# Kernel tuning notes

Hardware: AMD Instinct MI355X
Metric: run time of the kernel (lower is better)

## Reference

```python
import jax, jax.numpy as jnp
import numpy as np

N = 20000    # num nodes
E = 320000   # num edges (also rows of edge_type, SPN line-graph style)
F = 64       # num_features
HID = 64     # hidden_channels
HEADS = 4    # gatv2_heads
NC = 2       # num_classes
PH = 128     # proxy hidden size
SLOPE = 0.2  # PyG GATv2 leaky_relu negative slope


def gatv2(feat, src, dst, wl, wr, att, b, num_nodes, concat):
    # GATv2Conv (PyG semantics, add_self_loops=True, dropout off in eval)
    H, C = att.shape
    xl = (feat @ wl).reshape(-1, H, C)
    xr = (feat @ wr).reshape(-1, H, C)
    loops = jnp.arange(num_nodes, dtype=src.dtype)
    s = jnp.concatenate([src, loops])
    d = jnp.concatenate([dst, loops])
    e = jax.nn.leaky_relu(xl[s] + xr[d], SLOPE)            # [E', H, C]
    logits = jnp.einsum('ehc,hc->eh', e, att)              # [E', H]
    m = jax.ops.segment_max(logits, d, num_segments=num_nodes)
    p = jnp.exp(logits - m[d])
    z = jax.ops.segment_sum(p, d, num_segments=num_nodes)
    alpha = p / z[d]                                       # segment softmax
    out = jax.ops.segment_sum(xl[s] * alpha[:, :, None], d, num_segments=num_nodes)
    out = out.reshape(num_nodes, H * C) if concat else out.mean(axis=1)
    return out + b


def setup_inputs():
    key = jax.random.key(0)
    ks = iter(jax.random.split(key, 32))
    def rn(shape, scale=0.1):
        return jax.random.normal(next(ks), shape, dtype=jnp.float32) * scale
    return {
        'x': rn((N, F), 1.0),
        'edge_type': rn((E, F), 1.0),
        'edge_index': jax.random.randint(next(ks), (2, E), 0, N, dtype=jnp.int32),
        'n1_wl': rn((F, HEADS * HID)), 'n1_wr': rn((F, HEADS * HID)),
        'n1_att': rn((HEADS, HID)), 'n1_b': jnp.zeros((HEADS * HID,), jnp.float32),
        'n2_wl': rn((HEADS * HID, HID)), 'n2_wr': rn((HEADS * HID, HID)),
        'n2_att': rn((1, HID)), 'n2_b': jnp.zeros((HID,), jnp.float32),
        'e1_wl': rn((F, HEADS * HID)), 'e1_wr': rn((F, HEADS * HID)),
        'e1_att': rn((HEADS, HID)), 'e1_b': jnp.zeros((HEADS * HID,), jnp.float32),
        'e2_wl': rn((HEADS * HID, HID)), 'e2_wr': rn((HEADS * HID, HID)),
        'e2_att': rn((1, HID)), 'e2_b': jnp.zeros((HID,), jnp.float32),
        'crf_wu': rn((HID, NC)), 'crf_bu': jnp.zeros((NC,), jnp.float32),
        'crf_wp': rn((HID, NC)),
        'px_w1': rn((HID, PH)), 'px_b1': jnp.zeros((PH,), jnp.float32),
        'px_w2': rn((PH, NC)), 'px_b2': jnp.zeros((NC,), jnp.float32),
    }


def reference(x, edge_type, edge_index, n1_wl, n1_wr, n1_att, n1_b, n2_wl, n2_wr, n2_att, n2_b,
              e1_wl, e1_wr, e1_att, e1_b, e2_wl, e2_wr, e2_att, e2_b,
              crf_wu, crf_bu, crf_wp, px_w1, px_b1, px_w2, px_b2):
    src, dst = edge_index[0], edge_index[1]
    # node GNN: GATv2 -> ELU -> GATv2 (dropout = identity in eval)
    h = jax.nn.elu(gatv2(x, src, dst, n1_wl, n1_wr, n1_att, n1_b, N, True))
    node_repr = gatv2(h, src, dst, n2_wl, n2_wr, n2_att, n2_b, N, False)
    # edge GNN over edge features (E rows, same edge_index, per source code)
    g = jax.nn.elu(gatv2(edge_type, src, dst, e1_wl, e1_wr, e1_att, e1_b, E, True))
    edge_repr = gatv2(g, src, dst, e2_wl, e2_wr, e2_att, e2_b, E, False)
    # CRF head: unary potentials + pairwise messages scattered to dst nodes
    unary = node_repr @ crf_wu + crf_bu
    msg = jax.ops.segment_sum(edge_repr @ crf_wp, dst, num_segments=N)
    crf_out = jax.nn.log_softmax(unary + msg, axis=-1)
    # MLP proxy head
    ph = jax.nn.relu(node_repr @ px_w1 + px_b1)
    proxy_out = ph @ px_w2 + px_b2
    return crf_out, proxy_out
```

## Files before the change

### kernel.cpp

```cpp
#include <hip/hip_runtime.h>
#include <cstddef>
#include <cstdint>

#define N_NODES 20000
#define N_EDGES 320000

typedef __attribute__((ext_vector_type(8))) short bf8_t;
typedef __attribute__((ext_vector_type(4))) float f4_t;
typedef __attribute__((ext_vector_type(2))) float f2_t;
typedef unsigned short bfu;
typedef _Float16 half_t;
typedef __attribute__((ext_vector_type(2))) _Float16 h2_t;
typedef __attribute__((ext_vector_type(4))) _Float16 h4_t;
typedef __attribute__((ext_vector_type(8))) _Float16 h8_t;

__device__ __forceinline__ short f2bf(float f) {
  unsigned u = __float_as_uint(f);
  u += 0x7fff + ((u >> 16) & 1);
  return (short)(u >> 16);
}
__device__ __forceinline__ h2_t abs_h2(h2_t t) {
  unsigned u = __builtin_bit_cast(unsigned, t) & 0x7fff7fffu;
  return __builtin_bit_cast(h2_t, u);
}
__device__ __forceinline__ float dot2h(h2_t a, h2_t b, float c) {
#if __has_builtin(__builtin_amdgcn_fdot2)
  return __builtin_amdgcn_fdot2(a, b, c, false);
#else
  return c + (float)a.x * (float)b.x + (float)a.y * (float)b.y;
#endif
}

__global__ void count_deg_kernel(const int* __restrict__ dst, int* __restrict__ deg, int e_cnt) {
  int e = blockIdx.x * blockDim.x + threadIdx.x;
  if (e < e_cnt) atomicAdd(&deg[dst[e]], 1);
}

__global__ __launch_bounds__(1024) void scan_kernel(
    const int* __restrict__ deg, int* __restrict__ rowptr,
    int* __restrict__ cursor, int n) {
  __shared__ int sdata[1024];
  constexpr int CH = (N_NODES + 1023) / 1024;
  int tid = threadIdx.x;
  int base = tid * CH;
  int loc[CH];
  int s = 0;
  #pragma unroll
  for (int j = 0; j < CH; ++j) {
    int idx = base + j;
    int v = (idx < n) ? deg[idx] : 0;
    loc[j] = s;
    s += v;
  }
  sdata[tid] = s;
  __syncthreads();
  for (int off = 1; off < 1024; off <<= 1) {
    int t = (tid >= off) ? sdata[tid - off] : 0;
    __syncthreads();
    sdata[tid] += t;
    __syncthreads();
  }
  int excl = sdata[tid] - s;
  #pragma unroll
  for (int j = 0; j < CH; ++j) {
    int idx = base + j;
    if (idx < n) { int val = excl + loc[j]; rowptr[idx] = val; cursor[idx] = val; }
  }
  if (tid == 0) rowptr[n] = sdata[1023];
}

__global__ void fill_csr_kernel(const int* __restrict__ src, const int* __restrict__ dst,
                                int* __restrict__ cursor, int* __restrict__ csr_src,
                                int* __restrict__ csr_eid, int e_cnt) {
  int e = blockIdx.x * blockDim.x + threadIdx.x;
  if (e < e_cnt) {
    int pos = atomicAdd(&cursor[dst[e]], 1);
    csr_src[pos] = src[e];
    csr_eid[pos] = e;
  }
}

__global__ void prep_all_kernel(
    const float* __restrict__ n1l, const float* __restrict__ n1r,
    const float* __restrict__ e1l, const float* __restrict__ e1r,
    const float* __restrict__ n2l, const float* __restrict__ n2r,
    const float* __restrict__ e2l, const float* __restrict__ e2r,
    const float* __restrict__ b2, const float* __restrict__ wp,
    short* __restrict__ t_n1l, short* __restrict__ t_n1r,
    short* __restrict__ t_e1l, short* __restrict__ t_e1r,
    short* __restrict__ t_n2l, short* __restrict__ t_n2r,
    short* __restrict__ t_e2l, short* __restrict__ t_e2r,
    float* __restrict__ wct, float* __restrict__ pc)
{
  int i = blockIdx.x * blockDim.x + threadIdx.x;
  int seg = i >> 14;
  int j = i & 16383;
  if (seg < 4) {
    const float* srcs[4] = {n1l, n1r, e1l, e1r};
    short* dsts[4] = {t_n1l, t_n1r, t_e1l, t_e1r};
    int n = j >> 6, k = j & 63;
    dsts[seg][n * 64 + k] = f2bf(srcs[seg][k * 256 + n]);
  } else if (seg < 8) {
    const float* srcs[4] = {n2l, n2r, e2l, e2r};
    short* dsts[4] = {t_n2l, t_n2r, t_e2l, t_e2r};
    int n = j >> 8, k = j & 255;
    dsts[seg - 4][n * 256 + k] = f2bf(srcs[seg - 4][k * 64 + n]);
  } else if (seg == 8) {
    if (j < 512) {
      int jj = j & 1;
      int k  = j >> 1;
      float s = 0.f;
      for (int c = 0; c < 64; ++c) s = fmaf(e2l[k * 64 + c], wp[c * 2 + jj], s);
      wct[jj * 256 + k] = s;
    } else if (j < 514) {
      int jj = j - 512;
      float s = 0.f;
      for (int c = 0; c < 64; ++c) s = fmaf(b2[c], wp[c * 2 + jj], s);
      pc[jj] = s;
    }
  }
}

template<int K, typename SrcT>
__global__ __launch_bounds__(128) void mfma_proj2_kernel(
    const SrcT* __restrict__ A0,
    const short* __restrict__ Wtl0, const short* __restrict__ Wtr0,
    half_t* __restrict__ xl0, half_t* __restrict__ xr0,
    const SrcT* __restrict__ A1,
    const short* __restrict__ Wtl1, const short* __restrict__ Wtr1,
    half_t* __restrict__ xl1, half_t* __restrict__ xr1,
    const float* __restrict__ att0, const float* __restrict__ att1,
    float* __restrict__ ll0, float* __restrict__ lr0,
    float* __restrict__ ll1, float* __restrict__ lr1,
    int M, int nslices)
{
  constexpr int KC = K / 32;
  int tid = threadIdx.x;
  int w = tid >> 6, lane = tid & 63, quad = lane >> 4, l15 = lane & 15;
  int row_base = (int)blockIdx.x * 64 + w * 32;
  int y = (int)blockIdx.y;
  int z = (int)blockIdx.z;
  const SrcT* A = z ? A1 : A0;
  bool is_l = y < nslices;
  const short* Wt = z ? (is_l ? Wtl1 : Wtr1) : (is_l ? Wtl0 : Wtr0);
  half_t* dst = z ? (is_l ? xl1 : xr1) : (is_l ? xl0 : xr0);
  const float* att = z ? att1 : att0;
  float* lin = z ? (is_l ? ll1 : lr1) : (is_l ? ll0 : lr0);
  int head = is_l ? y : y - nslices;
  int cb = head * 64;
  const float* atp = att + head * 64;
  int STR = nslices * 64;

  bf8_t a[2][KC];
  #pragma unroll
  for (int rt = 0; rt < 2; ++rt) {
    int r = row_base + rt * 16 + l15;
    int rc = r < M ? r : M - 1;
    const SrcT* ap = A + (size_t)rc * K + quad * 8;
    #pragma unroll
    for (int kc = 0; kc < KC; ++kc) {
      bf8_t f;
      if constexpr (sizeof(SrcT) == 4) {
        float4 v0 = *(const float4*)(ap + kc * 32);
        float4 v1 = *(const float4*)(ap + kc * 32 + 4);
        f[0] = f2bf(v0.x); f[1] = f2bf(v0.y); f[2] = f2bf(v0.z); f[3] = f2bf(v0.w);
        f[4] = f2bf(v1.x); f[5] = f2bf(v1.y); f[6] = f2bf(v1.z); f[7] = f2bf(v1.w);
      } else {
        h8_t hv = *(const h8_t*)(ap + kc * 32);
        #pragma unroll
        for (int q = 0; q < 8; ++q) f[q] = f2bf((float)hv[q]);
      }
      a[rt][kc] = f;
    }
  }

  float lacc0 = 0.f, lacc1 = 0.f;
  #pragma unroll
  for (int nt = 0; nt < 4; ++nt) {
    f4_t acc0 = {0.f, 0.f, 0.f, 0.f};
    f4_t acc1 = {0.f, 0.f, 0.f, 0.f};
    const short* wb = Wt + (size_t)(cb + nt * 16 + l15) * K + quad * 8;
    #pragma unroll
    for (int kc = 0; kc < KC; ++kc) {
      bf8_t wf = *(const bf8_t*)(wb + kc * 32);
      acc0 = __builtin_amdgcn_mfma_f32_16x16x32_bf16(wf, a[0][kc], acc0, 0, 0, 0);
      acc1 = __builtin_amdgcn_mfma_f32_16x16x32_bf16(wf, a[1][kc], acc1, 0, 0, 0);
    }
    f4_t av = *(const f4_t*)(atp + nt * 16 + quad * 4);
    lacc0 += acc0[0] * av[0] + acc0[1] * av[1] + acc0[2] * av[2] + acc0[3] * av[3];
    lacc1 += acc1[0] * av[0] + acc1[1] * av[1] + acc1[2] * av[2] + acc1[3] * av[3];
    #pragma unroll
    for (int rt = 0; rt < 2; ++rt) {
      f4_t acc = rt == 0 ? acc0 : acc1;
      int row = row_base + rt * 16 + l15;
      if (row >= M) continue;
      int col = cb + nt * 16 + quad * 4;
      h4_t pk;
      pk[0] = (_Float16)acc[0]; pk[1] = (_Float16)acc[1];
      pk[2] = (_Float16)acc[2]; pk[3] = (_Float16)acc[3];
      *(h4_t*)&dst[(size_t)row * STR + col] = pk;
    }
  }
  lacc0 += __shfl_xor(lacc0, 16, 64); lacc0 += __shfl_xor(lacc0, 32, 64);
  lacc1 += __shfl_xor(lacc1, 16, 64); lacc1 += __shfl_xor(lacc1, 32, 64);
  if (quad == 0) {
    int r0 = row_base + l15;
    int r1 = row_base + 16 + l15;
    if (r0 < M) lin[(size_t)r0 * nslices + head] = 0.6f * lacc0;
    if (r1 < M) lin[(size_t)r1 * nslices + head] = 0.6f * lacc1;
  }
}

template<int KIN>
__device__ __forceinline__ void gemm_body(
    const float* __restrict__ A, const float* __restrict__ W, int wld, int cb,
    int block_m, int M, float (&acc)[8][4],
    float (*As)[128 + 4], float (*Ws)[64 + 4])
{
  int tid = threadIdx.x;
  int tx = tid & 15;
  int ty = tid >> 4;
  #pragma unroll
  for (int i = 0; i < 8; ++i)
    #pragma unroll
    for (int j = 0; j < 4; ++j) acc[i][j] = 0.f;

  for (int k0 = 0; k0 < KIN; k0 += 16) {
    #pragma unroll
    for (int rep = 0; rep < 2; ++rep) {
      int ar = (tid >> 2) + rep * 64;
      int ak = (tid & 3) * 4;
      int gr = block_m + ar;
      float4 v = make_float4(0.f, 0.f, 0.f, 0.f);
      if (gr < M) v = *(const float4*)&A[(size_t)gr * KIN + k0 + ak];
      As[ak + 0][ar] = v.x; As[ak + 1][ar] = v.y;
      As[ak + 2][ar] = v.z; As[ak + 3][ar] = v.w;
    }
    {
      int wr = tid >> 4;
      int wc = (tid & 15) * 4;
      float4 v = *(const float4*)&W[(size_t)(k0 + wr) * wld + cb + wc];
      Ws[wr][wc + 0] = v.x; Ws[wr][wc + 1] = v.y;
      Ws[wr][wc + 2] = v.z; Ws[wr][wc + 3] = v.w;
    }
    __syncthreads();
    #pragma unroll
    for (int k = 0; k < 16; ++k) {
      float a[8], w[4];
      #pragma unroll
      for (int i = 0; i < 8; ++i) a[i] = As[k][ty * 8 + i];
      #pragma unroll
      for (int j = 0; j < 4; ++j) w[j] = Ws[k][tx * 4 + j];
      #pragma unroll
      for (int i = 0; i < 8; ++i)
        #pragma unroll
        for (int j = 0; j < 4; ++j) acc[i][j] = fmaf(a[i], w[j], acc[i][j]);
    }
    __syncthreads();
  }
}

template<int KIN, int MODE>
__global__ __launch_bounds__(256) void gemm64_kernel(
    const float* __restrict__ A, const float* __restrict__ W, int wld,
    const float* __restrict__ bias, float* __restrict__ out, int old, int M)
{
  __shared__ float As[16][128 + 4];
  __shared__ float Ws[16][64 + 4];
  float acc[8][4];
  int block_m = (int)blockIdx.x * 128;
  int cb = (int)blockIdx.y * 64;
  gemm_body<KIN>(A, W, wld, cb, block_m, M, acc, As, Ws);

  int tid = threadIdx.x;
  int tx = tid & 15, ty = tid >> 4;
  int gc = cb + tx * 4;
  #pragma unroll
  for (int i = 0; i < 8; ++i) {
    int gr = block_m + ty * 8 + i;
    if (gr >= M) continue;
    size_t idx = (size_t)gr * old + gc;
    float t0 = acc[i][0], t1 = acc[i][1], t2 = acc[i][2], t3 = acc[i][3];
    if (MODE == 3) {
      t0 = fmaxf(t0 + bias[gc + 0], 0.f);
      t1 = fmaxf(t1 + bias[gc + 1], 0.f);
      t2 = fmaxf(t2 + bias[gc + 2], 0.f);
      t3 = fmaxf(t3 + bias[gc + 3], 0.f);
    }
    *(float4*)&out[idx] = make_float4(t0, t1, t2, t3);
  }
}

__global__ __launch_bounds__(256) void gat_agg_l1(
    const half_t* __restrict__ xl0, const half_t* __restrict__ xr0,
    const float* __restrict__ att0, const float* __restrict__ bias0,
    half_t* __restrict__ out0,
    const half_t* __restrict__ xl1, const half_t* __restrict__ xr1,
    const float* __restrict__ att1, const float* __restrict__ bias1,
    half_t* __restrict__ out1,
    const float* __restrict__ ll0, const float* __restrict__ lr0,
    const float* __restrict__ ll1, const float* __restrict__ lr1,
    const int* __restrict__ rowptr, const int* __restrict__ csr_src)
{
  constexpr int GRP = N_NODES / 4;
  int tid = threadIdx.x;
  int w = tid >> 6, lane = tid & 63;
  int egrp = lane >> 5;
  int head = (lane >> 3) & 3;
  int coff = (lane & 31) * 8;
  int bid = (int)blockIdx.x;
  int chain = bid >= GRP ? 1 : 0;
  int d = (bid - chain * GRP) * 4 + w;

  const half_t* xl = chain ? xl1 : xl0;
  const half_t* xr = chain ? xr1 : xr0;
  const float* att = chain ? att1 : att0;
  const float* bias = chain ? bias1 : bias0;
  const float* linl = chain ? ll1 : ll0;
  const float* linr = chain ? lr1 : lr0;
  half_t* out = chain ? out1 : out0;

  int row0 = rowptr[d];
  int deg = rowptr[d + 1] - row0;

  h2_t xr2[4], attA[4];
  {
    h8_t xv = *(const h8_t*)&xr[(unsigned)(d * 256 + coff)];
    xr2[0] = h2_t{xv[0], xv[1]}; xr2[1] = h2_t{xv[2], xv[3]};
    xr2[2] = h2_t{xv[4], xv[5]}; xr2[3] = h2_t{xv[6], xv[7]};
    const float* atp = att + coff;
    float4 b0 = *(const float4*)(atp);
    float4 b1 = *(const float4*)(atp + 4);
    attA[0] = h2_t{(_Float16)(0.4f * b0.x), (_Float16)(0.4f * b0.y)};
    attA[1] = h2_t{(_Float16)(0.4f * b0.z), (_Float16)(0.4f * b0.w)};
    attA[2] = h2_t{(_Float16)(0.4f * b1.x), (_Float16)(0.4f * b1.y)};
    attA[3] = h2_t{(_Float16)(0.4f * b1.z), (_Float16)(0.4f * b1.w)};
  }
  float linr_d = linr[(unsigned)(d * 4 + head)];

  auto ld_idx = [&](int k) -> int {
    int idx = k * 2 + egrp;
    int cl = idx < deg ? idx : (deg > 0 ? deg - 1 : 0);
    int pos = deg > 0 ? row0 + cl : 0;
    int sv = csr_src[pos];
    return idx < deg ? sv : d;
  };

  float zloc, a8[8];
  {
    h8_t xu = *(const h8_t*)&xl[(unsigned)(d * 256 + coff)];
    float part = 0.f;
    #pragma unroll
    for (int j = 0; j < 4; ++j) {
      h2_t t = h2_t{xu[2 * j], xu[2 * j + 1]} + xr2[j];
      part = dot2h(abs_h2(t), attA[j], part);
    }
    part += __shfl_xor(part, 1, 64);
    part += __shfl_xor(part, 2, 64);
    part += __shfl_xor(part, 4, 64);
    part += linl[(unsigned)(d * 4 + head)] + linr_d;
    float wgt = __expf(part);
    float ws = (egrp == 0) ? wgt : 0.f;
    zloc = ws;
    #pragma unroll
    for (int i = 0; i < 8; ++i) a8[i] = (float)xu[i] * ws;
  }

  int C = (deg + 1) >> 1;
  int s_cur = ld_idx(0);
  h8_t xu_cur = *(const h8_t*)&xl[(unsigned)(s_cur * 256 + coff)];
  float lin_cur = linl[(unsigned)(s_cur * 4 + head)];
  int s_nxt = ld_idx(1);
  for (int k = 0; k < C; ++k) {
    h8_t xu_nxt = *(const h8_t*)&xl[(unsigned)(s_nxt * 256 + coff)];
    float lin_nxt = linl[(unsigned)(s_nxt * 4 + head)];
    int s_n2 = ld_idx(k + 2);
    bool valid = (k * 2 + egrp) < deg;
    float part = 0.f;
    #pragma unroll
    for (int j = 0; j < 4; ++j) {
      h2_t t = h2_t{xu_cur[2 * j], xu_cur[2 * j + 1]} + xr2[j];
      part = dot2h(abs_h2(t), attA[j], part);
    }
    part += __shfl_xor(part, 1, 64);
    part += __shfl_xor(part, 2, 64);
    part += __shfl_xor(part, 4, 64);
    part += lin_cur + linr_d;
    float wgt = valid ? __expf(part) : 0.f;
    zloc += wgt;
    #pragma unroll
    for (int i = 0; i < 8; ++i) a8[i] = fmaf((float)xu_cur[i], wgt, a8[i]);
    xu_cur = xu_nxt; lin_cur = lin_nxt; s_nxt = s_n2;
  }

  zloc += __shfl_xor(zloc, 32, 64);
  #pragma unroll
  for (int i = 0; i < 8; ++i) a8[i] += __shfl_xor(a8[i], 32, 64);

  if (egrp == 0) {
    float invz = 1.f / zloc;
    const float* bp = bias + coff;
    float4 c0 = *(const float4*)(bp);
    float4 c1 = *(const float4*)(bp + 4);
    float o[8];
    o[0] = a8[0] * invz + c0.x; o[1] = a8[1] * invz + c0.y;
    o[2] = a8[2] * invz + c0.z; o[3] = a8[3] * invz + c0.w;
    o[4] = a8[4] * invz + c1.x; o[5] = a8[5] * invz + c1.y;
    o[6] = a8[6] * invz + c1.z; o[7] = a8[7] * invz + c1.w;
    #pragma unroll
    for (int i = 0; i < 8; ++i) o[i] = o[i] > 0.f ? o[i] : __expf(o[i]) - 1.f;
    h8_t pk;
    #pragma unroll
    for (int i = 0; i < 8; ++i) pk[i] = (_Float16)o[i];
    *(h8_t*)&out[(size_t)d * 256 + coff] = pk;
  }
}

__global__ __launch_bounds__(256) void gat_agg_l2(
    const half_t* __restrict__ xl0, const half_t* __restrict__ xr0,
    const float* __restrict__ att0, const float* __restrict__ bias0,
    float* __restrict__ out0,
    const half_t* __restrict__ xl1, const half_t* __restrict__ xr1,
    const float* __restrict__ att1, const float* __restrict__ bias1,
    const float* __restrict__ ll0, const float* __restrict__ lr0,
    const float* __restrict__ ll1, const float* __restrict__ lr1,
    const int* __restrict__ rowptr, const int* __restrict__ csr_src,
    const float* __restrict__ wp, float* __restrict__ pbuf)
{
  constexpr int GRP = N_NODES / 4;
  int tid = threadIdx.x;
  int w = tid >> 6;
  int lane = tid & 63;
  int egrp = lane >> 3;
  int cch  = lane & 7;
  int bid = (int)blockIdx.x;
  int chain = bid >= GRP ? 1 : 0;
  int d = (bid - chain * GRP) * 4 + w;

  const half_t* xl = chain ? xl1 : xl0;
  const half_t* xr = chain ? xr1 : xr0;
  const float* att = chain ? att1 : att0;
  const float* bias = chain ? bias1 : bias0;
  const float* linl = chain ? ll1 : ll0;
  const float* linr = chain ? lr1 : lr0;

  int row0 = rowptr[d];
  int deg = rowptr[d + 1] - row0;
  int cbase = cch * 8;

  h2_t xr2[4], attA[4];
  {
    h8_t xv = *(const h8_t*)&xr[(unsigned)(d * 64 + cbase)];
    xr2[0] = h2_t{xv[0], xv[1]}; xr2[1] = h2_t{xv[2], xv[3]};
    xr2[2] = h2_t{xv[4], xv[5]}; xr2[3] = h2_t{xv[6], xv[7]};
    const float* atp = att + cbase;
    float4 b0 = *(const float4*)(atp);
    float4 b1 = *(const float4*)(atp + 4);
    attA[0] = h2_t{(_Float16)(0.4f * b0.x), (_Float16)(0.4f * b0.y)};
    attA[1] = h2_t{(_Float16)(0.4f * b0.z), (_Float16)(0.4f * b0.w)};
    attA[2] = h2_t{(_Float16)(0.4f * b1.x), (_Float16)(0.4f * b1.y)};
    attA[3] = h2_t{(_Float16)(0.4f * b1.z), (_Float16)(0.4f * b1.w)};
  }
  float linr_d = linr[d];

  auto ld_idx = [&](int k) -> int {
    int idx = k * 8 + egrp;
    int cl = idx < deg ? idx : (deg > 0 ? deg - 1 : 0);
    int pos = deg > 0 ? row0 + cl : 0;
    int sv = csr_src[pos];
    return idx < deg ? sv : d;
  };

  float zloc, a8[8];
  {
    h8_t xu = *(const h8_t*)&xl[(unsigned)(d * 64 + cbase)];
    float part = 0.f;
    #pragma unroll
    for (int j = 0; j < 4; ++j) {
      h2_t t = h2_t{xu[2 * j], xu[2 * j + 1]} + xr2[j];
      part = dot2h(abs_h2(t), attA[j], part);
    }
    part += __shfl_xor(part, 1, 64);
    part += __shfl_xor(part, 2, 64);
    part += __shfl_xor(part, 4, 64);
    part += linl[d] + linr_d;
    float wgt = __expf(part);
    float ws = (egrp == 0) ? wgt : 0.f;
    zloc = ws;
    #pragma unroll
    for (int i = 0; i < 8; ++i) a8[i] = (float)xu[i] * ws;
  }

  int C = (deg + 7) >> 3;
  int s_cur = ld_idx(0);
  h8_t xu_cur = *(const h8_t*)&xl[(unsigned)(s_cur * 64 + cbase)];
  float lin_cur = linl[s_cur];
  int s_nxt = ld_idx(1);
  for (int k = 0; k < C; ++k) {
    h8_t xu_nxt = *(const h8_t*)&xl[(unsigned)(s_nxt * 64 + cbase)];
    float lin_nxt = linl[s_nxt];
    int s_n2 = ld_idx(k + 2);
    bool valid = (k * 8 + egrp) < deg;
    float part = 0.f;
    #pragma unroll
    for (int j = 0; j < 4; ++j) {
      h2_t t = h2_t{xu_cur[2 * j], xu_cur[2 * j + 1]} + xr2[j];
      part = dot2h(abs_h2(t), attA[j], part);
    }
    part += __shfl_xor(part, 1, 64);
    part += __shfl_xor(part, 2, 64);
    part += __shfl_xor(part, 4, 64);
    part += lin_cur + linr_d;
    float wgt = valid ? __expf(part) : 0.f;
    zloc += wgt;
    #pragma unroll
    for (int i = 0; i < 8; ++i) a8[i] = fmaf((float)xu_cur[i], wgt, a8[i]);
    xu_cur = xu_nxt; lin_cur = lin_nxt; s_nxt = s_n2;
  }

  #pragma unroll
  for (int off = 8; off < 64; off <<= 1) {
    zloc += __shfl_xor(zloc, off, 64);
    #pragma unroll
    for (int i = 0; i < 8; ++i) a8[i] += __shfl_xor(a8[i], off, 64);
  }

  float invz = 1.f / zloc;
  float o[8];
  #pragma unroll
  for (int i = 0; i < 8; ++i) o[i] = a8[i] * invz + bias[cbase + i];

  if (chain) {
    float p0 = 0.f, p1 = 0.f;
    #pragma unroll
    for (int i = 0; i < 8; ++i) {
      float2 wv = *(const float2*)&wp[(cbase + i) * 2];
      p0 = fmaf(o[i], wv.x, p0);
      p1 = fmaf(o[i], wv.y, p1);
    }
    p0 += __shfl_xor(p0, 1, 64); p1 += __shfl_xor(p1, 1, 64);
    p0 += __shfl_xor(p0, 2, 64); p1 += __shfl_xor(p1, 2, 64);
    p0 += __shfl_xor(p0, 4, 64); p1 += __shfl_xor(p1, 4, 64);
    if (lane == 0) *(float2*)&pbuf[2 * d] = make_float2(p0, p1);
  } else if (egrp == 0) {
    float* op = out0 + (size_t)d * 64 + cbase;
    *(float4*)(op)     = make_float4(o[0], o[1], o[2], o[3]);
    *(float4*)(op + 4) = make_float4(o[4], o[5], o[6], o[7]);
  }
}

__global__ __launch_bounds__(256) void chunk_fold_kernel(
    const float* __restrict__ A,
    const short* __restrict__ W1t,
    const float* __restrict__ b1,
    const float* __restrict__ WcT,
    const float* __restrict__ pc,
    float* __restrict__ pbufN,
    int Mtot)
{
  __shared__ short Ws[256 * 72];
  __shared__ float b1s[256];
  __shared__ float wcs[512];

  int tid = threadIdx.x;
  int w = tid >> 6;
  int lane = tid & 63;
  int quad = lane >> 4;
  int l15 = lane & 15;
  int row_base = (int)blockIdx.x * 256 + w * 64;

  #pragma unroll
  for (int j = 0; j < 8; ++j) {
    int g = j * 256 + tid;
    int row = g >> 3, c = g & 7;
    *(int4*)&Ws[row * 72 + c * 8] = *(const int4*)&W1t[(size_t)g * 8];
  }
  b1s[tid] = b1[tid];
  wcs[tid] = WcT[tid];
  wcs[256 + tid] = WcT[256 + tid];
  __syncthreads();

  bf8_t a1[4][2];
  #pragma unroll
  for (int rt = 0; rt < 4; ++rt) {
    int r = row_base + rt * 16 + l15;
    int rc = r < Mtot ? r : Mtot - 1;
    const float* ap = A + (size_t)rc * 64 + quad * 8;
    #pragma unroll
    for (int ks = 0; ks < 2; ++ks) {
      float4 v0 = *(const float4*)(ap + ks * 32);
      float4 v1 = *(const float4*)(ap + ks * 32 + 4);
      bf8_t f;
      f[0] = f2bf(v0.x); f[1] = f2bf(v0.y); f[2] = f2bf(v0.z); f[3] = f2bf(v0.w);
      f[4] = f2bf(v1.x); f[5] = f2bf(v1.y); f[6] = f2bf(v1.z); f[7] = f2bf(v1.w);
      a1[rt][ks] = f;
    }
  }

  float p0[4] = {0.f, 0.f, 0.f, 0.f};
  float p1[4] = {0.f, 0.f, 0.f, 0.f};

  #pragma unroll
  for (int i = 0; i < 16; ++i) {
    const short* wl = &Ws[(i * 16 + l15) * 72 + quad * 8];
    bf8_t w0 = *(const bf8_t*)(wl);
    bf8_t w1 = *(const bf8_t*)(wl + 32);

    f4_t g[4];
    #pragma unroll
    for (int rt = 0; rt < 4; ++rt) {
      f4_t z = {0.f, 0.f, 0.f, 0.f};
      z = __builtin_amdgcn_mfma_f32_16x16x32_bf16(w0, a1[rt][0], z, 0, 0, 0);
      z = __builtin_amdgcn_mfma_f32_16x16x32_bf16(w1, a1[rt][1], z, 0, 0, 0);
      g[rt] = z;
    }
    int cbase = i * 16 + quad * 4;
    f4_t b4  = *(const f4_t*)&b1s[cbase];
    f4_t wc0 = *(const f4_t*)&wcs[cbase];
    f4_t wc1 = *(const f4_t*)&wcs[256 + cbase];
    #pragma unroll
    for (int rt = 0; rt < 4; ++rt) {
      #pragma unroll
      for (int r = 0; r < 4; ++r) {
        float v = g[rt][r] + b4[r];
        v = v > 0.f ? v : __expf(v) - 1.f;
        p0[rt] = fmaf(v, wc0[r], p0[rt]);
        p1[rt] = fmaf(v, wc1[r], p1[rt]);
      }
    }
  }

  #pragma unroll
  for (int off = 16; off < 64; off <<= 1) {
    #pragma unroll
    for (int rt = 0; rt < 4; ++rt) {
      p0[rt] += __shfl_xor(p0[rt], off, 64);
      p1[rt] += __shfl_xor(p1[rt], off, 64);
    }
  }
  if (quad == 0) {
    float c0 = pc[0], c1 = pc[1];
    #pragma unroll
    for (int rt = 0; rt < 4; ++rt) {
      int row = row_base + rt * 16 + l15;
      if (row < Mtot)
        *(float2*)&pbufN[2 * row] = make_float2(p0[rt] + c0, p1[rt] + c1);
    }
  }
}

__global__ void head_kernel(const float* __restrict__ node_repr, const float* __restrict__ ph,
                            const int* __restrict__ rowptr, const int* __restrict__ csr_eid,
                            const float* __restrict__ pbuf, const float* __restrict__ wu,
                            const float* __restrict__ bu, const float* __restrict__ w2,
                            const float* __restrict__ b2, float* __restrict__ out, int n) {
  __shared__ float swu[128];
  __shared__ float sw2[256];
  int tid = threadIdx.x;
  if (tid < 128) swu[tid] = wu[tid];
  sw2[tid] = w2[tid];
  __syncthreads();
  int i = blockIdx.x * blockDim.x + tid;
  if (i >= n) return;
  float m0 = 0.f, m1 = 0.f;
  int r0 = rowptr[i], r1 = rowptr[i + 1];
  int jj = r0;
  for (; jj + 4 <= r1; jj += 4) {
    int e0 = csr_eid[jj + 0], e1 = csr_eid[jj + 1];
    int e2 = csr_eid[jj + 2], e3 = csr_eid[jj + 3];
    float2 q0 = *(const float2*)&pbuf[2 * e0];
    float2 q1 = *(const float2*)&pbuf[2 * e1];
    float2 q2 = *(const float2*)&pbuf[2 * e2];
    float2 q3 = *(const float2*)&pbuf[2 * e3];
    m0 += (q0.x + q1.x) + (q2.x + q3.x);
    m1 += (q0.y + q1.y) + (q2.y + q3.y);
  }
  for (; jj < r1; ++jj) {
    int e = csr_eid[jj];
    float2 q = *(const float2*)&pbuf[2 * e];
    m0 += q.x; m1 += q.y;
  }
  const float* nr = node_repr + (size_t)i * 64;
  float u0 = bu[0], u1 = bu[1];
  #pragma unroll
  for (int k = 0; k < 64; ++k) {
    float v = nr[k];
    u0 = fmaf(v, swu[2 * k + 0], u0);
    u1 = fmaf(v, swu[2 * k + 1], u1);
  }
  float v0 = u0 + m0;
  float v1 = u1 + m1;
  float mx = fmaxf(v0, v1);
  float lse = mx + logf(__expf(v0 - mx) + __expf(v1 - mx));
  out[2 * i + 0] = v0 - lse;
  out[2 * i + 1] = v1 - lse;
  const float* p = ph + (size_t)i * 128;
  float p0 = b2[0], p1 = b2[1];
  #pragma unroll
  for (int k = 0; k < 128; ++k) {
    float v = p[k];
    p0 = fmaf(v, sw2[2 * k + 0], p0);
    p1 = fmaf(v, sw2[2 * k + 1], p1);
  }
  out[2 * n + 2 * i + 0] = p0;
  out[2 * n + 2 * i + 1] = p1;
}

extern "C" void kernel_launch(void* const* d_in, const int* in_sizes, int n_in,
                              void* d_out, int out_size, void* d_ws, size_t ws_size,
                              hipStream_t stream) {
  const int N = N_NODES, E = N_EDGES;
  const float* x         = (const float*)d_in[0];
  const float* edge_type = (const float*)d_in[1];
  const int*   ei        = (const int*)d_in[2];
  const float* n1_wl  = (const float*)d_in[3];
  const float* n1_wr  = (const float*)d_in[4];
  const float* n1_att = (const float*)d_in[5];
  const float* n1_b   = (const float*)d_in[6];
  const float* n2_wl  = (const float*)d_in[7];
  const float* n2_wr  = (const float*)d_in[8];
  const float* n2_att = (const float*)d_in[9];
  const float* n2_b   = (const float*)d_in[10];
  const float* e1_wl  = (const float*)d_in[11];
  const float* e1_wr  = (const float*)d_in[12];
  const float* e1_att = (const float*)d_in[13];
  const float* e1_b   = (const float*)d_in[14];
  const float* e2_wl  = (const float*)d_in[15];
  const float* e2_wr  = (const float*)d_in[16];
  const float* e2_att = (const float*)d_in[17];
  const float* e2_b   = (const float*)d_in[18];
  const float* crf_wu = (const float*)d_in[19];
  const float* crf_bu = (const float*)d_in[20];
  const float* crf_wp = (const float*)d_in[21];
  const float* px_w1  = (const float*)d_in[22];
  const float* px_b1  = (const float*)d_in[23];
  const float* px_w2  = (const float*)d_in[24];
  const float* px_b2  = (const float*)d_in[25];
  float* out = (float*)d_out;
  const int* src = ei;
  const int* dst = ei + E;
  (void)in_sizes; (void)n_in; (void)out_size; (void)ws_size;

  char* ws = (char*)d_ws;
  size_t off = 0;
  auto alloc = [&](size_t bytes) -> void* {
    void* p = ws + off;
    off += (bytes + 255) & ~(size_t)255;
    return p;
  };
  half_t* xl_n  = (half_t*)alloc((size_t)N * 256 * 2);
  half_t* xr_n  = (half_t*)alloc((size_t)N * 256 * 2);
  half_t* xl_e  = (half_t*)alloc((size_t)N * 256 * 2);
  half_t* xr_e  = (half_t*)alloc((size_t)N * 256 * 2);
  half_t* h_n  = (half_t*)alloc((size_t)N * 256 * 4);
  half_t* g_e  = (half_t*)alloc((size_t)N * 256 * 4);
  half_t* xl2_n = (half_t*)alloc((size_t)N * 64 * 2);
  half_t* xr2_n = (half_t*)alloc((size_t)N * 64 * 2);
  half_t* xl2_e = (half_t*)alloc((size_t)N * 64 * 2);
  half_t* xr2_e = (half_t*)alloc((size_t)N * 64 * 2);
  float* B3    = (float*)alloc((size_t)N * 64 * 4);
  float* pbuf  = (float*)alloc((size_t)E * 2 * 4);
  float* ph    = (float*)(void*)xl_n;
  int* deg     = (int*)alloc((size_t)N * 4);
  int* rowptr  = (int*)alloc((size_t)(N + 1) * 4);
  int* cursor  = (int*)alloc((size_t)N * 4);
  int* csr_src = (int*)alloc((size_t)E * 4);
  int* csr_eid = (int*)alloc((size_t)E * 4);
  short* t_n1l = (short*)alloc((size_t)16384 * 2);
  short* t_n1r = (short*)alloc((size_t)16384 * 2);
  short* t_e1l = (short*)alloc((size_t)16384 * 2);
  short* t_e1r = (short*)alloc((size_t)16384 * 2);
  short* t_n2l = (short*)alloc((size_t)16384 * 2);
  short* t_n2r = (short*)alloc((size_t)16384 * 2);
  short* t_e2l = (short*)alloc((size_t)16384 * 2);
  short* t_e2r = (short*)alloc((size_t)16384 * 2);
  float* WcT   = (float*)alloc((size_t)2 * 256 * 4);
  float* pcv   = (float*)alloc((size_t)2 * 4);
  float* l1ln = pbuf;
  float* l1rn = pbuf + 80000;
  float* l1le = pbuf + 160000;
  float* l1re = pbuf + 240000;
  float* l2base = (float*)(void*)xr_n;
  float* l2ln = l2base;
  float* l2rn = l2base + 20000;
  float* l2le = l2base + 40000;
  float* l2re = l2base + 60000;

  const int EB = (E + 255) / 256;
  const int NB = (N + 127) / 128;
  const int PB = (N + 63) / 64;
  const int Mhigh = E - N;
  const int CFB = (Mhigh + 255) / 256;
  const int GRP = N / 4;

  hipMemsetAsync(deg, 0, (size_t)N * 4, stream);
  count_deg_kernel<<<EB, 256, 0, stream>>>(dst, deg, E);
  scan_kernel<<<1, 1024, 0, stream>>>(deg, rowptr, cursor, N);
  fill_csr_kernel<<<EB, 256, 0, stream>>>(src, dst, cursor, csr_src, csr_eid, E);
  prep_all_kernel<<<515, 256, 0, stream>>>(n1_wl, n1_wr, e1_wl, e1_wr,
                                           n2_wl, n2_wr, e2_wl, e2_wr,
                                           e2_b, crf_wp,
                                           t_n1l, t_n1r, t_e1l, t_e1r,
                                           t_n2l, t_n2r, t_e2l, t_e2r, WcT, pcv);

  mfma_proj2_kernel<64, float><<<dim3(PB, 8, 2), 128, 0, stream>>>(
      x, t_n1l, t_n1r, xl_n, xr_n,
      edge_type, t_e1l, t_e1r, xl_e, xr_e,
      n1_att, e1_att, l1ln, l1rn, l1le, l1re, N, 4);
  gat_agg_l1<<<2 * GRP, 256, 0, stream>>>(
      xl_n, xr_n, n1_att, n1_b, h_n,
      xl_e, xr_e, e1_att, e1_b, g_e,
      l1ln, l1rn, l1le, l1re, rowptr, csr_src);

  mfma_proj2_kernel<256, half_t><<<dim3(PB, 2, 2), 128, 0, stream>>>(
      h_n, t_n2l, t_n2r, xl2_n, xr2_n,
      g_e, t_e2l, t_e2r, xl2_e, xr2_e,
      n2_att, e2_att, l2ln, l2rn, l2le, l2re, N, 1);
  gat_agg_l2<<<2 * GRP, 256, 0, stream>>>(
      xl2_n, xr2_n, n2_att, n2_b, B3,
      xl2_e, xr2_e, e2_att, e2_b,
      l2ln, l2rn, l2le, l2re, rowptr, csr_src, crf_wp, pbuf);

  chunk_fold_kernel<<<CFB, 256, 0, stream>>>(edge_type + (size_t)N * 64, t_e1l,
                                             e1_b, WcT, pcv, pbuf + 2 * (size_t)N, Mhigh);

  gemm64_kernel<64, 3><<<dim3(NB, 2), 256, 0, stream>>>(B3, px_w1, 128, px_b1, ph, 128, N);
  head_kernel<<<(N + 255) / 256, 256, 0, stream>>>(B3, ph, rowptr, csr_eid, pbuf,
                                                   crf_wu, crf_bu, px_w2, px_b2, out, N);
}
```

Measured before the change: 397.8 us.

## Schedule aggregation nodes in descending-degree order via counting sort

Adds a degree histogram, a scan and a scatter pass that build a permutation of nodes sorted by descending in-degree. Both GAT aggregation kernels then process destination nodes in that order, so heavy nodes start first and the tail of the launch is better balanced. The cost is three extra small kernel launches plus a memset, and the loss of locality between neighbouring destination ids within a block. The order buffer reuses the cursor array and the histogram reuses B3, both of which must already be free at those points.

```diff
diff --git a/kernel.cpp b/kernel.cpp
--- a/kernel.cpp
+++ b/kernel.cpp
@@ -77,6 +77,39 @@
     int pos = atomicAdd(&cursor[dst[e]], 1);
     csr_src[pos] = src[e];
     csr_eid[pos] = e;
+  }
+}
+
+__global__ void deg_hist_kernel(const int* __restrict__ deg, int* __restrict__ hist, int n) {
+  int i = blockIdx.x * blockDim.x + threadIdx.x;
+  if (i < n) {
+    int b = deg[i]; b = b > 511 ? 511 : b;
+    atomicAdd(&hist[511 - b], 1);
+  }
+}
+
+__global__ __launch_bounds__(512) void hist_scan_kernel(
+    const int* __restrict__ hist, int* __restrict__ hcur) {
+  __shared__ int s[512];
+  int t = threadIdx.x;
+  s[t] = hist[t];
+  __syncthreads();
+  for (int off = 1; off < 512; off <<= 1) {
+    int v = (t >= off) ? s[t - off] : 0;
+    __syncthreads();
+    s[t] += v;
+    __syncthreads();
+  }
+  hcur[t] = s[t] - hist[t];
+}
+
+__global__ void order_scatter_kernel(const int* __restrict__ deg, int* __restrict__ hcur,
+                                     int* __restrict__ order, int n) {
+  int i = blockIdx.x * blockDim.x + threadIdx.x;
+  if (i < n) {
+    int b = deg[i]; b = b > 511 ? 511 : b;
+    int pos = atomicAdd(&hcur[511 - b], 1);
+    order[pos] = i;
   }
 }
 
@@ -300,7 +333,8 @@
     half_t* __restrict__ out1,
     const float* __restrict__ ll0, const float* __restrict__ lr0,
     const float* __restrict__ ll1, const float* __restrict__ lr1,
-    const int* __restrict__ rowptr, const int* __restrict__ csr_src)
+    const int* __restrict__ rowptr, const int* __restrict__ csr_src,
+    const int* __restrict__ order)
 {
   constexpr int GRP = N_NODES / 4;
   int tid = threadIdx.x;
@@ -310,7 +344,7 @@
   int coff = (lane & 31) * 8;
   int bid = (int)blockIdx.x;
   int chain = bid >= GRP ? 1 : 0;
-  int d = (bid - chain * GRP) * 4 + w;
+  int d = order[(bid - chain * GRP) * 4 + w];
 
   const half_t* xl = chain ? xl1 : xl0;
   const half_t* xr = chain ? xr1 : xr0;
@@ -425,7 +459,8 @@
     const float* __restrict__ ll0, const float* __restrict__ lr0,
     const float* __restrict__ ll1, const float* __restrict__ lr1,
     const int* __restrict__ rowptr, const int* __restrict__ csr_src,
-    const float* __restrict__ wp, float* __restrict__ pbuf)
+    const float* __restrict__ wp, float* __restrict__ pbuf,
+    const int* __restrict__ order)
 {
   constexpr int GRP = N_NODES / 4;
   int tid = threadIdx.x;
@@ -435,7 +470,7 @@
   int cch  = lane & 7;
   int bid = (int)blockIdx.x;
   int chain = bid >= GRP ? 1 : 0;
-  int d = (bid - chain * GRP) * 4 + w;
+  int d = order[(bid - chain * GRP) * 4 + w];
 
   const half_t* xl = chain ? xl1 : xl0;
   const half_t* xr = chain ? xr1 : xr0;
@@ -785,18 +820,26 @@
   float* l2rn = l2base + 20000;
   float* l2le = l2base + 40000;
   float* l2re = l2base + 60000;
+  int* hist  = (int*)(void*)B3;
+  int* hcur  = hist + 512;
+  int* order = cursor;
 
   const int EB = (E + 255) / 256;
   const int NB = (N + 127) / 128;
   const int PB = (N + 63) / 64;
+  const int NB256 = (N + 255) / 256;
   const int Mhigh = E - N;
   const int CFB = (Mhigh + 255) / 256;
   const int GRP = N / 4;
 
   hipMemsetAsync(deg, 0, (size_t)N * 4, stream);
+  hipMemsetAsync(hist, 0, 512 * 4, stream);
   count_deg_kernel<<<EB, 256, 0, stream>>>(dst, deg, E);
   scan_kernel<<<1, 1024, 0, stream>>>(deg, rowptr, cursor, N);
   fill_csr_kernel<<<EB, 256, 0, stream>>>(src, dst, cursor, csr_src, csr_eid, E);
+  deg_hist_kernel<<<NB256, 256, 0, stream>>>(deg, hist, N);
+  hist_scan_kernel<<<1, 512, 0, stream>>>(hist, hcur);
+  order_scatter_kernel<<<NB256, 256, 0, stream>>>(deg, hcur, order, N);
   prep_all_kernel<<<515, 256, 0, stream>>>(n1_wl, n1_wr, e1_wl, e1_wr,
                                            n2_wl, n2_wr, e2_wl, e2_wr,
                                            e2_b, crf_wp,
@@ -810,7 +853,7 @@
   gat_agg_l1<<<2 * GRP, 256, 0, stream>>>(
       xl_n, xr_n, n1_att, n1_b, h_n,
       xl_e, xr_e, e1_att, e1_b, g_e,
-      l1ln, l1rn, l1le, l1re, rowptr, csr_src);
+      l1ln, l1rn, l1le, l1re, rowptr, csr_src, order);
 
   mfma_proj2_kernel<256, half_t><<<dim3(PB, 2, 2), 128, 0, stream>>>(
       h_n, t_n2l, t_n2r, xl2_n, xr2_n,
@@ -819,7 +862,7 @@
   gat_agg_l2<<<2 * GRP, 256, 0, stream>>>(
       xl2_n, xr2_n, n2_att, n2_b, B3,
       xl2_e, xr2_e, e2_att, e2_b,
-      l2ln, l2rn, l2le, l2re, rowptr, csr_src, crf_wp, pbuf);
+      l2ln, l2rn, l2le, l2re, rowptr, csr_src, crf_wp, pbuf, order);
 
   chunk_fold_kernel<<<CFB, 256, 0, stream>>>(edge_type + (size_t)N * 64, t_e1l,
                                              e1_b, WcT, pcv, pbuf + 2 * (size_t)N, Mhigh);
```

Result: slower. 515.1 us (+29.5%).
